# Optimization experiments

Measured on AMD Instinct MI355X. Metric: run time of the kernel, lower is better.

Reference implementation:

```python
import jax, jax.numpy as jnp
import numpy as np

N = 50000


def gcn_conv(x, edge_index, W, b):
    # PyG GCNConv: h = XW; add self-loops; sym-normalized scatter-add; + bias
    n = x.shape[0]
    h = x @ W  # [N, out]
    loop = jnp.arange(n)
    src = jnp.concatenate([edge_index[0], loop])
    dst = jnp.concatenate([edge_index[1], loop])
    deg = jax.ops.segment_sum(jnp.ones_like(dst, dtype=h.dtype), dst, num_segments=n)
    dinv = jax.lax.rsqrt(jnp.maximum(deg, 1.0))  # deg >= 1 after self-loops
    norm = dinv[src] * dinv[dst]  # [E+N]
    msg = h[src] * norm[:, None]  # [E+N, out]
    return jax.ops.segment_sum(msg, dst, num_segments=n) + b


def setup_inputs() -> dict:
    key = jax.random.key(0)
    ks = jax.random.split(key, 20)
    E = 1600000
    inp = {
        "metadata_a": jax.random.normal(ks[0], (N, 512), jnp.float32),
        "metadata_b": jax.random.normal(ks[1], (N, 512), jnp.float32),
        "x_a": jax.random.normal(ks[2], (N, 256), jnp.float32),
        "x_b": jax.random.normal(ks[3], (N, 256), jnp.float32),
        "edge_index_a": jax.random.randint(ks[4], (2, E), 0, N, dtype=jnp.int64),
        "edge_index_b": jax.random.randint(ks[5], (2, E), 0, N, dtype=jnp.int64),
        # parameters (fan-in scaled)
        "fc1_W": jax.random.normal(ks[6], (512, 128), jnp.float32) / np.sqrt(512),
        "fc1_b": jnp.zeros((128,), jnp.float32),
        "fc2_W": jax.random.normal(ks[7], (128, 128), jnp.float32) / np.sqrt(128),
        "fc2_b": jnp.zeros((128,), jnp.float32),
        "gcn1_W": jax.random.normal(ks[8], (256, 128), jnp.float32) / np.sqrt(256),
        "gcn1_b": jnp.zeros((128,), jnp.float32),
        "gcn2_W": jax.random.normal(ks[9], (128, 128), jnp.float32) / np.sqrt(128),
        "gcn2_b": jnp.zeros((128,), jnp.float32),
        "fcc_W": jax.random.normal(ks[10], (512, 128), jnp.float32) / np.sqrt(512),
        "fcc_b": jnp.zeros((128,), jnp.float32),
        "out_W": jax.random.normal(ks[11], (128, 1), jnp.float32) / np.sqrt(128),
        "out_b": jnp.zeros((1,), jnp.float32),
    }
    return inp


def reference(metadata_a, metadata_b, x_a, x_b, edge_index_a, edge_index_b,
              fc1_W, fc1_b, fc2_W, fc2_b, gcn1_W, gcn1_b, gcn2_W, gcn2_b,
              fcc_W, fcc_b, out_W, out_b):
    def mlp(m):
        m = jax.nn.relu(m @ fc1_W + fc1_b)
        return jax.nn.relu(m @ fc2_W + fc2_b)

    def gcn_branch(x, ei):
        x = jax.nn.relu(gcn_conv(x, ei, gcn1_W, gcn1_b))
        return jax.nn.relu(gcn_conv(x, ei, gcn2_W, gcn2_b))

    ma = mlp(metadata_a)
    mb = mlp(metadata_b)
    ga = gcn_branch(x_a, edge_index_a)
    gb = gcn_branch(x_b, edge_index_b)
    combined = jnp.concatenate([ma, mb, ga, gb], axis=1)  # [N, 512]
    combined = jax.nn.relu(combined @ fcc_W + fcc_b)
    return jax.nn.sigmoid(combined @ out_W + out_b)  # [N, 1]
```

## Files before the change

### kernel.cpp

```cpp
#include <hip/hip_runtime.h>
#include <math.h>


typedef __attribute__((ext_vector_type(8))) short bf16x8;
typedef __attribute__((ext_vector_type(4))) float f32x4;

static __device__ __forceinline__ unsigned short f2bf(float f) {
  unsigned u = __float_as_uint(f);
  unsigned r = u + 0x7fffu + ((u >> 16) & 1u);
  return (unsigned short)(r >> 16);
}
static __device__ __forceinline__ float bflo(unsigned m) { return __uint_as_float(m << 16); }
static __device__ __forceinline__ float bfhi(unsigned m) { return __uint_as_float(m & 0xffff0000u); }

static __device__ __forceinline__ bf16x8 cvt8(const float4& l, const float4& h) {
  bf16x8 a;
  a[0] = (short)f2bf(l.x); a[1] = (short)f2bf(l.y);
  a[2] = (short)f2bf(l.z); a[3] = (short)f2bf(l.w);
  a[4] = (short)f2bf(h.x); a[5] = (short)f2bf(h.y);
  a[6] = (short)f2bf(h.z); a[7] = (short)f2bf(h.w);
  return a;
}

static __device__ __forceinline__ void gl_lds16(const unsigned short* g, unsigned short* l) {
  __builtin_amdgcn_global_load_lds(
      (const __attribute__((address_space(1))) void*)g,
      (__attribute__((address_space(3))) void*)l, 16, 0, 0);
}

template <int KT>
__launch_bounds__(256)
__global__ void gemm_staged(const float* __restrict__ Av, const float* __restrict__ Av2,
                            int lda, const unsigned short* __restrict__ Wt,
                            const float* __restrict__ bias, const float* __restrict__ rowscale,
                            unsigned short* __restrict__ Cb, unsigned short* __restrict__ Cb2,
                            int ldc, int co, int co2, int Mh, int M, int do_relu) {
  static_assert(KT % 4 == 0, "KT multiple of 4");
  constexpr int NCH = KT / 4;
  __shared__ float4 As[2][2048];
  const int tid = threadIdx.x;
  const int wave = tid >> 6, lane = tid & 63, quad = lane >> 4, lr = lane & 15;
  const int m0 = blockIdx.x * 64 + wave * 16;
  const int mb = blockIdx.x * 64;

  f32x4 acc[8];
#pragma unroll
  for (int c = 0; c < 8; c++) acc[c] = (f32x4){0.f, 0.f, 0.f, 0.f};

  const int colq_src = (tid & 7) ^ ((tid >> 3) & 7);
  int r0g = mb + (tid >> 3);      if (r0g > M - 1) r0g = M - 1;
  int r1g = mb + 32 + (tid >> 3); if (r1g > M - 1) r1g = M - 1;
  const int h0 = r0g >= Mh, h1 = r1g >= Mh;
  const float* srcb0 = (h0 ? Av2 : Av) + (size_t)(r0g - (h0 ? Mh : 0)) * lda + colq_src * 4;
  const float* srcb1 = (h1 ? Av2 : Av) + (size_t)(r1g - (h1 ? Mh : 0)) * lda + colq_src * 4;

  auto stage = [&](int buf, int c0) {
#pragma unroll
    for (int s = 0; s < 8; s++) {
      const float* g = ((s & 1) ? srcb1 : srcb0) + (size_t)(c0 * 4 + (s >> 1)) * 32;
      gl_lds16((const unsigned short*)g,
               (unsigned short*)&As[buf][s * 256 + wave * 64]);
    }
  };

  const int h32 = wave >> 1;
  const int r5 = (wave & 1) * 16 + lr;
  const int swz = r5 & 7;
  const int fb_ = h32 * 256 + r5 * 8;

  const bf16x8* Bf = (const bf16x8*)Wt + lane;

  stage(0, 0);
  bf16x8 bb[2][8];
#pragma unroll
  for (int c = 0; c < 8; c++) bb[0][c] = Bf[c * 64];
  __builtin_amdgcn_sched_barrier(0);
  asm volatile("s_waitcnt vmcnt(0)" ::: "memory");
  __builtin_amdgcn_s_barrier();
  __builtin_amdgcn_sched_barrier(0);

  for (int ch = 0; ch < NCH; ch++) {
    if (ch + 1 < NCH) stage((ch + 1) & 1, ch + 1);
    const float4* cur = As[ch & 1];
#pragma unroll
    for (int kk = 0; kk < 4; kk++) {
      const int kt = ch * 4 + kk;
      float4 f0 = cur[kk * 512 + fb_ + ((2 * quad) ^ swz)];
      float4 f1 = cur[kk * 512 + fb_ + ((2 * quad + 1) ^ swz)];
      bf16x8 a = cvt8(f0, f1);
      if (kt + 1 < KT) {
        const bf16x8* Bk = Bf + (size_t)(kt + 1) * 512;
#pragma unroll
        for (int c = 0; c < 8; c++) bb[(kk + 1) & 1][c] = Bk[c * 64];
      }
#pragma unroll
      for (int c = 0; c < 8; c++)
        acc[c] = __builtin_amdgcn_mfma_f32_16x16x32_bf16(a, bb[kk & 1][c], acc[c], 0, 0, 0);
    }
    if (ch + 1 < NCH) {
      __builtin_amdgcn_sched_barrier(0);
      asm volatile("s_waitcnt vmcnt(0)" ::: "memory");
      __builtin_amdgcn_s_barrier();
      __builtin_amdgcn_sched_barrier(0);
    }
  }

  const int rbase = m0 + quad * 4;
  float rs[4];
#pragma unroll
  for (int i = 0; i < 4; i++) {
    int row = rbase + i;
    rs[i] = (rowscale && row < M) ? rowscale[row] : 1.0f;
  }
#pragma unroll
  for (int c = 0; c < 8; c++) {
    const int nc = c * 16 + lr;
    const float bi = bias ? bias[nc] : 0.f;
#pragma unroll
    for (int i = 0; i < 4; i++) {
      int row = rbase + i;
      if (row < M) {
        int hh = row >= Mh;
        int rr = row - (hh ? Mh : 0);
        float v = acc[c][i] * rs[i] + bi;
        if (do_relu) v = fmaxf(v, 0.f);
        unsigned short* C = hh ? Cb2 : Cb;
        C[(size_t)rr * ldc + (hh ? co2 : co) + nc] = f2bf(v);
      }
    }
  }
}

__launch_bounds__(256)
__global__ void gemm_reg4(const unsigned short* __restrict__ Av, const unsigned short* __restrict__ Av2,
                          int lda, const unsigned short* __restrict__ Wt,
                          const float* __restrict__ bias, const float* __restrict__ rowscale,
                          unsigned short* __restrict__ Cb, unsigned short* __restrict__ Cb2,
                          int ldc, int co, int co2, int Mh, int M, int do_relu) {
  const int tid = threadIdx.x;
  const int wave = tid >> 6, lane = tid & 63, quad = lane >> 4, lr = lane & 15;
  const int m0 = blockIdx.x * 64 + wave * 16;

  f32x4 acc[8];
#pragma unroll
  for (int c = 0; c < 8; c++) acc[c] = (f32x4){0.f, 0.f, 0.f, 0.f};

  int rg = m0 + lr; if (rg > M - 1) rg = M - 1;
  const int h = rg >= Mh;
  const unsigned short* aph = (h ? Av2 : Av) + (size_t)(rg - (h ? Mh : 0)) * lda + quad * 8;
  const bf16x8* Bf = (const bf16x8*)Wt + lane;

  bf16x8 hb[4];
#pragma unroll
  for (int k = 0; k < 4; k++) hb[k] = *(const bf16x8*)(aph + (size_t)k * 32);

  bf16x8 bb[2][8];
#pragma unroll
  for (int c = 0; c < 8; c++) bb[0][c] = Bf[c * 64];

#pragma unroll
  for (int kt = 0; kt < 4; kt++) {
    if (kt + 1 < 4) {
      const bf16x8* Bk = Bf + (size_t)(kt + 1) * 512;
#pragma unroll
      for (int c = 0; c < 8; c++) bb[(kt + 1) & 1][c] = Bk[c * 64];
    }
#pragma unroll
    for (int c = 0; c < 8; c++)
      acc[c] = __builtin_amdgcn_mfma_f32_16x16x32_bf16(hb[kt], bb[kt & 1][c], acc[c], 0, 0, 0);
  }

  const int rbase = m0 + quad * 4;
  float rs[4];
#pragma unroll
  for (int i = 0; i < 4; i++) {
    int row = rbase + i;
    rs[i] = (rowscale && row < M) ? rowscale[row] : 1.0f;
  }
#pragma unroll
  for (int c = 0; c < 8; c++) {
    const int nc = c * 16 + lr;
    const float bi = bias ? bias[nc] : 0.f;
#pragma unroll
    for (int i = 0; i < 4; i++) {
      int row = rbase + i;
      if (row < M) {
        int hh = row >= Mh;
        int rr = row - (hh ? Mh : 0);
        float v = acc[c][i] * rs[i] + bi;
        if (do_relu) v = fmaxf(v, 0.f);
        unsigned short* C = hh ? Cb2 : Cb;
        C[(size_t)rr * ldc + (hh ? co2 : co) + nc] = f2bf(v);
      }
    }
  }
}

__launch_bounds__(256)
__global__ void gemm_head(const unsigned short* __restrict__ A,
                          const unsigned short* __restrict__ Wt,
                          const float* __restrict__ bias,
                          const float* __restrict__ outW, const float* __restrict__ outb,
                          float* __restrict__ y, int M) {
  constexpr int KT = 16;
  const int tid = threadIdx.x;
  const int wave = tid >> 6, lane = tid & 63, quad = lane >> 4, lr = lane & 15;
  const int m0 = blockIdx.x * 64 + wave * 16;

  f32x4 acc[8];
#pragma unroll
  for (int c = 0; c < 8; c++) acc[c] = (f32x4){0.f, 0.f, 0.f, 0.f};

  int rg = m0 + lr; if (rg > M - 1) rg = M - 1;
  const unsigned short* aph = A + (size_t)rg * 512 + quad * 8;
  const bf16x8* Bf = (const bf16x8*)Wt + lane;

  bf16x8 hb[2][4];
#define LOADH(SLOT, BT)                                                     \
  if ((BT) < 4) {                                                           \
    _Pragma("unroll")                                                       \
    for (int kk = 0; kk < 4; kk++)                                          \
      hb[SLOT][kk] = *(const bf16x8*)(aph + (size_t)((BT) * 4 + kk) * 32);  \
  }
  LOADH(0, 0)
  LOADH(1, 1)

  bf16x8 bb[2][8];
#pragma unroll
  for (int c = 0; c < 8; c++) bb[0][c] = Bf[c * 64];

#pragma unroll
  for (int bt = 0; bt < 4; bt++) {
#pragma unroll
    for (int kk = 0; kk < 4; kk++) {
      const int kt = bt * 4 + kk;
      bf16x8 a = hb[bt & 1][kk];
      if (kt + 1 < KT) {
        const bf16x8* Bk = Bf + (size_t)(kt + 1) * 512;
#pragma unroll
        for (int c = 0; c < 8; c++) bb[(kk + 1) & 1][c] = Bk[c * 64];
      }
      if (kk == 3) { LOADH(bt & 1, bt + 2) }
#pragma unroll
      for (int c = 0; c < 8; c++)
        acc[c] = __builtin_amdgcn_mfma_f32_16x16x32_bf16(a, bb[kk & 1][c], acc[c], 0, 0, 0);
    }
  }
#undef LOADH

  float part[4] = {0.f, 0.f, 0.f, 0.f};
#pragma unroll
  for (int c = 0; c < 8; c++) {
    const int nc = c * 16 + lr;
    float w = outW[nc];
    float bi = bias[nc];
#pragma unroll
    for (int i = 0; i < 4; i++) part[i] += fmaxf(acc[c][i] + bi, 0.f) * w;
  }
#pragma unroll
  for (int i = 0; i < 4; i++) {
    part[i] += __shfl_xor(part[i], 1, 64);
    part[i] += __shfl_xor(part[i], 2, 64);
    part[i] += __shfl_xor(part[i], 4, 64);
    part[i] += __shfl_xor(part[i], 8, 64);
  }
  if (lr == 0) {
    const float ob = outb[0];
#pragma unroll
    for (int i = 0; i < 4; i++) {
      int row = m0 + quad * 4 + i;
      if (row < M) y[row] = 1.f / (1.f + expf(-(part[i] + ob)));
    }
  }
}

__global__ void prep_w(const float* __restrict__ fc1, const float* __restrict__ fc2,
                       const float* __restrict__ g1, const float* __restrict__ g2,
                       const float* __restrict__ fcc, unsigned short* __restrict__ wt) {
  int t = blockIdx.x * 256 + threadIdx.x;
  const float* src[5] = {fc1, fc2, g1, g2, fcc};
  const int Ks[5] = {512, 128, 256, 128, 512};
  int off = 0;
#pragma unroll
  for (int w = 0; w < 5; w++) {
    int K = Ks[w];
    int ngroups = K * 16;
    if (t < ngroups) {
      int lane = t & 63;
      int c = (t >> 6) & 7;
      int kt = t >> 9;
      int quad = lane >> 4, lr = lane & 15;
      int n = c * 16 + lr;
      unsigned short* dst = wt + off + (size_t)t * 8;
      const float* s = src[w];
#pragma unroll
      for (int j = 0; j < 8; j++) {
        int k = kt * 32 + quad * 8 + j;
        dst[j] = f2bf(s[k * 128 + n]);
      }
    }
    off += K * 128;
  }
}

__global__ void init_csr(int* __restrict__ gcur, int NB, int BCAP) {
  int i = blockIdx.x * 256 + threadIdx.x;
  if (i < 2 * NB) gcur[i] = i * BCAP;
}

__launch_bounds__(256)
__global__ void bucket_scatter(const int* __restrict__ eiA, const int* __restrict__ eiB,
                               int E, int T, int NB, int* __restrict__ gcur,
                               unsigned* __restrict__ records) {
  __shared__ unsigned staging[4096];
  __shared__ int hist[129];
  __shared__ int offs[129];
  __shared__ int gbase[128];
  __shared__ int sm[128];
  const int g = blockIdx.x >= T;
  const int tile = blockIdx.x - g * T;
  const int* ei = g ? eiB : eiA;
  const int tid = threadIdx.x;
  for (int i = tid; i <= NB; i += 256) hist[i] = 0;
  __syncthreads();
  const int base = tile * 4096;
  int myb[16], myp[16];
  unsigned myrec[16];
#pragma unroll
  for (int j = 0; j < 16; j++) {
    int li = base + j * 256 + tid;
    int b = NB;
    unsigned rec = 0;
    if (li < E) {
      int s = ei[li], d = ei[E + li];
      b = d >> 9;
      rec = (unsigned)s | ((unsigned)d << 16);
    }
    myb[j] = b; myrec[j] = rec;
    myp[j] = atomicAdd(&hist[b], 1);
  }
  __syncthreads();
  if (tid < 128) sm[tid] = (tid <= NB) ? hist[tid] : 0;
  __syncthreads();
  for (int d = 1; d < 128; d <<= 1) {
    int v = 0;
    if (tid < 128) { v = sm[tid]; if (tid >= d) v += sm[tid - d]; }
    __syncthreads();
    if (tid < 128) sm[tid] = v;
    __syncthreads();
  }
  if (tid < 128) offs[tid] = sm[tid] - ((tid <= NB) ? hist[tid] : 0);
  __syncthreads();
#pragma unroll
  for (int j = 0; j < 16; j++)
    if (myb[j] < NB) staging[offs[myb[j]] + myp[j]] = myrec[j];
  if (tid < NB && hist[tid] > 0) gbase[tid] = atomicAdd(&gcur[g * NB + tid], hist[tid]);
  __syncthreads();
  const int total = offs[NB];
  for (int i = tid; i < total; i += 256) {
    unsigned rec = staging[i];
    int b = (int)(rec >> 16) >> 9;
    records[gbase[b] + (i - offs[b])] = rec;
  }
}

__launch_bounds__(256)
__global__ void csr_build(const unsigned* __restrict__ records, const int* __restrict__ gcur,
                          int N, int NB, int BCAP,
                          int2* __restrict__ rpA, int2* __restrict__ rpB,
                          float* __restrict__ dinv, unsigned short* __restrict__ csrAll) {
  __shared__ int ncnt[512];
  __shared__ int excl[512];
  __shared__ int sm[256];
  const int g = blockIdx.x >= NB;
  const int b = blockIdx.x - g * NB;
  const int tid = threadIdx.x;
  const int R = (g * NB + b) * BCAP;
  const int cnt = gcur[g * NB + b] - R;
  const int node0 = b << 9;
  const int nb = min(512, N - node0);
  const unsigned* rec = records + R;
  int2* rp = g ? rpB : rpA;
  unsigned short* csr = csrAll + (size_t)g * NB * BCAP;

  for (int i = tid; i < 512; i += 256) ncnt[i] = 0;
  __syncthreads();
  for (int i = tid; i < cnt; i += 256)
    atomicAdd(&ncnt[(rec[i] >> 16) & 511], 1);
  __syncthreads();
  int a0 = ncnt[2 * tid], a1 = ncnt[2 * tid + 1];
  int ps = a0 + a1;
  sm[tid] = ps;
  __syncthreads();
  for (int d = 1; d < 256; d <<= 1) {
    int v = sm[tid];
    if (tid >= d) v += sm[tid - d];
    __syncthreads();
    sm[tid] = v;
    __syncthreads();
  }
  int e0 = sm[tid] - ps;
  excl[2 * tid] = e0;
  excl[2 * tid + 1] = e0 + a0;
  __syncthreads();
  for (int i = tid; i < nb; i += 256) {
    int s = b * BCAP + excl[i];
    rp[node0 + i] = make_int2(s, s + ncnt[i]);
    dinv[g * N + node0 + i] = rsqrtf((float)(ncnt[i] + 1));
  }
  __syncthreads();
  for (int i = tid; i < 512; i += 256) ncnt[i] = excl[i];
  __syncthreads();
  for (int i = tid; i < cnt; i += 256) {
    unsigned r = rec[i];
    int p = atomicAdd(&ncnt[(r >> 16) & 511], 1);
    csr[b * BCAP + p] = (unsigned short)(r & 0xffffu);
  }
}

struct f2x4 { float2 a, b, c, d; };
static __device__ __forceinline__ void acc2(f2x4& A, const uint4& m) {
  A.a.x += bflo(m.x); A.a.y += bfhi(m.x);
  A.b.x += bflo(m.y); A.b.y += bfhi(m.y);
  A.c.x += bflo(m.z); A.c.y += bfhi(m.z);
  A.d.x += bflo(m.w); A.d.y += bfhi(m.w);
}

__launch_bounds__(256)
__global__ void gather16(const unsigned short* __restrict__ hsA,
                         const unsigned short* __restrict__ hsB,
                         const unsigned short* __restrict__ csrA,
                         const unsigned short* __restrict__ csrB,
                         const int2* __restrict__ rpA, const int2* __restrict__ rpB,
                         const float* __restrict__ dinv,
                         const float* __restrict__ bias,
                         unsigned short* __restrict__ outA, unsigned short* __restrict__ outB,
                         int ldA, int coA, int ldB, int coB, int N) {
  int widx = (blockIdx.x * 256 + threadIdx.x) >> 6;
  if (widx >= 2 * N) return;
  int g = widx >= N;
  int v = g ? widx - N : widx;
  const unsigned short* hs = g ? hsB : hsA;
  const unsigned short* csr = g ? csrB : csrA;
  int2 se = (g ? rpB : rpA)[v];
  unsigned short* out = g ? outB : outA;
  const int ldc = g ? ldB : ldA;
  const int co = g ? coB : coA;
  const int lane = threadIdx.x & 63;
  const int grp = lane >> 4;
  const int u = lane & 15;
  const unsigned short* rowb = hs + u * 8;

  f2x4 A0 = {{0,0},{0,0},{0,0},{0,0}};
  f2x4 A1 = {{0,0},{0,0},{0,0},{0,0}};

  int e = se.x;
  const int end = se.y;
  for (; e + 16 <= end; e += 16) {
    int s0 = csr[e + grp];
    int s1 = csr[e + 4 + grp];
    int s2 = csr[e + 8 + grp];
    int s3 = csr[e + 12 + grp];
    uint4 m0 = *(const uint4*)(rowb + (size_t)s0 * 128);
    uint4 m1 = *(const uint4*)(rowb + (size_t)s1 * 128);
    uint4 m2 = *(const uint4*)(rowb + (size_t)s2 * 128);
    uint4 m3 = *(const uint4*)(rowb + (size_t)s3 * 128);
    acc2(A0, m0); acc2(A1, m1); acc2(A0, m2); acc2(A1, m3);
  }
  for (; e + 4 <= end; e += 4) {
    int s0 = csr[e + grp];
    uint4 m0 = *(const uint4*)(rowb + (size_t)s0 * 128);
    acc2(A0, m0);
  }
  int r = end - e;
  if (r > 0) {
    int s0 = csr[e + (grp < r ? grp : r - 1)];
    uint4 m = *(const uint4*)(rowb + (size_t)s0 * 128);
    float msk = (grp < r) ? 1.f : 0.f;
    A1.a.x = fmaf(msk, bflo(m.x), A1.a.x); A1.a.y = fmaf(msk, bfhi(m.x), A1.a.y);
    A1.b.x = fmaf(msk, bflo(m.y), A1.b.x); A1.b.y = fmaf(msk, bfhi(m.y), A1.b.y);
    A1.c.x = fmaf(msk, bflo(m.z), A1.c.x); A1.c.y = fmaf(msk, bfhi(m.z), A1.c.y);
    A1.d.x = fmaf(msk, bflo(m.w), A1.d.x); A1.d.y = fmaf(msk, bfhi(m.w), A1.d.y);
  }

  float acc[8] = {A0.a.x + A1.a.x, A0.a.y + A1.a.y, A0.b.x + A1.b.x, A0.b.y + A1.b.y,
                  A0.c.x + A1.c.x, A0.c.y + A1.c.y, A0.d.x + A1.d.x, A0.d.y + A1.d.y};
#pragma unroll
  for (int j = 0; j < 8; j++) {
    acc[j] += __shfl_down(acc[j], 32, 64);
    acc[j] += __shfl_down(acc[j], 16, 64);
  }
  if (grp == 0) {
    uint4 smv = *(const uint4*)(rowb + (size_t)v * 128);
    acc[0] += bflo(smv.x); acc[1] += bfhi(smv.x);
    acc[2] += bflo(smv.y); acc[3] += bfhi(smv.y);
    acc[4] += bflo(smv.z); acc[5] += bfhi(smv.z);
    acc[6] += bflo(smv.w); acc[7] += bfhi(smv.w);
    float dv = dinv[g * N + v];
    float4 b0 = *(const float4*)(bias + u * 8);
    float4 b1 = *(const float4*)(bias + u * 8 + 4);
    float o0 = fmaxf(acc[0] * dv + b0.x, 0.f), o1 = fmaxf(acc[1] * dv + b0.y, 0.f);
    float o2 = fmaxf(acc[2] * dv + b0.z, 0.f), o3 = fmaxf(acc[3] * dv + b0.w, 0.f);
    float o4 = fmaxf(acc[4] * dv + b1.x, 0.f), o5 = fmaxf(acc[5] * dv + b1.y, 0.f);
    float o6 = fmaxf(acc[6] * dv + b1.z, 0.f), o7 = fmaxf(acc[7] * dv + b1.w, 0.f);
    uint4 P;
    P.x = (unsigned)f2bf(o0) | ((unsigned)f2bf(o1) << 16);
    P.y = (unsigned)f2bf(o2) | ((unsigned)f2bf(o3) << 16);
    P.z = (unsigned)f2bf(o4) | ((unsigned)f2bf(o5) << 16);
    P.w = (unsigned)f2bf(o6) | ((unsigned)f2bf(o7) << 16);
    *(uint4*)(out + (size_t)v * ldc + co + u * 8) = P;
  }
}

extern "C" void kernel_launch(void* const* d_in, const int* in_sizes, int n_in,
                              void* d_out, int out_size, void* d_ws, size_t ws_size,
                              hipStream_t stream) {
  const float* meta_a = (const float*)d_in[0];
  const float* meta_b = (const float*)d_in[1];
  const float* x_a    = (const float*)d_in[2];
  const float* x_b    = (const float*)d_in[3];
  const int*   ei_a   = (const int*)d_in[4];
  const int*   ei_b   = (const int*)d_in[5];
  const float* fc1_W = (const float*)d_in[6];
  const float* fc1_b = (const float*)d_in[7];
  const float* fc2_W = (const float*)d_in[8];
  const float* fc2_b = (const float*)d_in[9];
  const float* gcn1_W = (const float*)d_in[10];
  const float* gcn1_b = (const float*)d_in[11];
  const float* gcn2_W = (const float*)d_in[12];
  const float* gcn2_b = (const float*)d_in[13];
  const float* fcc_W = (const float*)d_in[14];
  const float* fcc_b = (const float*)d_in[15];
  const float* out_W = (const float*)d_in[16];
  const float* out_b = (const float*)d_in[17];
  float* y = (float*)d_out;

  const int N = in_sizes[0] / 512;
  const int E = in_sizes[4] / 2;
  const int NB = (N + 511) >> 9;
  const int T = (E + 4095) / 4096;
  const int BCAP = 17408;

  char* p = (char*)d_ws;
  auto alloc = [&](size_t bytes) { char* r = p; p += (bytes + 255) & ~255ull; return r; };
  unsigned short* combined = (unsigned short*)alloc((size_t)N * 512 * 2);
  unsigned short* t0 = (unsigned short*)alloc((size_t)N * 128 * 2);
  unsigned short* t1 = (unsigned short*)alloc((size_t)N * 128 * 2);
  unsigned short* t2 = (unsigned short*)alloc((size_t)N * 128 * 2);
  unsigned short* t3 = (unsigned short*)alloc((size_t)N * 128 * 2);
  unsigned short* wt = (unsigned short*)alloc(196608 * 2);
  float* dinv = (float*)alloc((size_t)2 * N * 4);
  int2* rpA = (int2*)alloc((size_t)N * 8);
  int2* rpB = (int2*)alloc((size_t)N * 8);
  int* gcur = (int*)alloc((size_t)2 * NB * 4);
  unsigned* records = (unsigned*)alloc((size_t)2 * NB * BCAP * 4 + 4096);
  unsigned short* csrAll = (unsigned short*)alloc((size_t)2 * NB * BCAP * 2 + 4096);
  unsigned short* csrA = csrAll;
  unsigned short* csrB = csrAll + (size_t)NB * BCAP;

  unsigned short* wt_fc1 = wt;
  unsigned short* wt_fc2 = wt + 65536;
  unsigned short* wt_g1  = wt + 81920;
  unsigned short* wt_g2  = wt + 114688;
  unsigned short* wt_fcc = wt + 131072;

  const int grid1 = (N + 63) / 64;
  const int grid2 = (2 * N + 63) / 64;

  prep_w<<<32, 256, 0, stream>>>(fc1_W, fc2_W, gcn1_W, gcn2_W, fcc_W, wt);
  init_csr<<<1, 256, 0, stream>>>(gcur, NB, BCAP);
  bucket_scatter<<<2 * T, 256, 0, stream>>>(ei_a, ei_b, E, T, NB, gcur, records);
  csr_build<<<2 * NB, 256, 0, stream>>>(records, gcur, N, NB, BCAP, rpA, rpB, dinv, csrAll);

  gemm_staged<16><<<grid2, 256, 0, stream>>>(meta_a, meta_b, 512, wt_fc1, fc1_b, nullptr,
                                             t0, t1, 128, 0, 0, N, 2 * N, 1);
  gemm_reg4<<<grid2, 256, 0, stream>>>(t0, t1, 128, wt_fc2, fc2_b, nullptr,
                                       combined, combined, 512, 0, 128, N, 2 * N, 1);

  gemm_staged<8><<<grid2, 256, 0, stream>>>(x_a, x_b, 256, wt_g1, nullptr, dinv,
                                            t0, t1, 128, 0, 0, N, 2 * N, 0);
  gather16<<<(2 * N + 3) / 4, 256, 0, stream>>>(t0, t1, csrA, csrB, rpA, rpB, dinv, gcn1_b,
                                                t2, t3, 128, 0, 128, 0, N);
  gemm_reg4<<<grid2, 256, 0, stream>>>(t2, t3, 128, wt_g2, nullptr, dinv,
                                       t0, t1, 128, 0, 0, N, 2 * N, 0);
  gather16<<<(2 * N + 3) / 4, 256, 0, stream>>>(t0, t1, csrA, csrB, rpA, rpB, dinv, gcn2_b,
                                                combined, combined, 512, 256, 512, 384, N);

  gemm_head<<<grid1, 256, 0, stream>>>(combined, wt_fcc, fcc_b, out_W, out_b, y, N);
}
```

Before: 745.8 us.

## Unify GEMMs into 128-row tile kernel staging weights in LDS

Replaces the two GEMM kernels with one templated kernel. Each wave now computes two 16-row tiles (128 rows per block). Weight chunks are staged into LDS via global_load_lds and shared across waves, while A rows are loaded straight into registers and prefetched one chunk ahead. This reuses each B fragment across two MFMA tiles and cuts global weight traffic per row, at the cost of more registers (launch bounds hint of 3 blocks) and fewer blocks in the grid.

```diff
diff --git a/kernel.cpp b/kernel.cpp
--- a/kernel.cpp
+++ b/kernel.cpp
@@ -28,169 +28,131 @@
       (__attribute__((address_space(3))) void*)l, 16, 0, 0);
 }
 
-template <int KT>
-__launch_bounds__(256)
-__global__ void gemm_staged(const float* __restrict__ Av, const float* __restrict__ Av2,
-                            int lda, const unsigned short* __restrict__ Wt,
-                            const float* __restrict__ bias, const float* __restrict__ rowscale,
-                            unsigned short* __restrict__ Cb, unsigned short* __restrict__ Cb2,
-                            int ldc, int co, int co2, int Mh, int M, int do_relu) {
-  static_assert(KT % 4 == 0, "KT multiple of 4");
-  constexpr int NCH = KT / 4;
-  __shared__ float4 As[2][2048];
-  const int tid = threadIdx.x;
-  const int wave = tid >> 6, lane = tid & 63, quad = lane >> 4, lr = lane & 15;
-  const int m0 = blockIdx.x * 64 + wave * 16;
-  const int mb = blockIdx.x * 64;
-
-  f32x4 acc[8];
-#pragma unroll
-  for (int c = 0; c < 8; c++) acc[c] = (f32x4){0.f, 0.f, 0.f, 0.f};
-
-  const int colq_src = (tid & 7) ^ ((tid >> 3) & 7);
-  int r0g = mb + (tid >> 3);      if (r0g > M - 1) r0g = M - 1;
-  int r1g = mb + 32 + (tid >> 3); if (r1g > M - 1) r1g = M - 1;
-  const int h0 = r0g >= Mh, h1 = r1g >= Mh;
-  const float* srcb0 = (h0 ? Av2 : Av) + (size_t)(r0g - (h0 ? Mh : 0)) * lda + colq_src * 4;
-  const float* srcb1 = (h1 ? Av2 : Av) + (size_t)(r1g - (h1 ? Mh : 0)) * lda + colq_src * 4;
-
-  auto stage = [&](int buf, int c0) {
-#pragma unroll
-    for (int s = 0; s < 8; s++) {
-      const float* g = ((s & 1) ? srcb1 : srcb0) + (size_t)(c0 * 4 + (s >> 1)) * 32;
-      gl_lds16((const unsigned short*)g,
-               (unsigned short*)&As[buf][s * 256 + wave * 64]);
-    }
-  };
-
-  const int h32 = wave >> 1;
-  const int r5 = (wave & 1) * 16 + lr;
-  const int swz = r5 & 7;
-  const int fb_ = h32 * 256 + r5 * 8;
-
-  const bf16x8* Bf = (const bf16x8*)Wt + lane;
-
-  stage(0, 0);
-  bf16x8 bb[2][8];
-#pragma unroll
-  for (int c = 0; c < 8; c++) bb[0][c] = Bf[c * 64];
-  __builtin_amdgcn_sched_barrier(0);
-  asm volatile("s_waitcnt vmcnt(0)" ::: "memory");
-  __builtin_amdgcn_s_barrier();
-  __builtin_amdgcn_sched_barrier(0);
-
-  for (int ch = 0; ch < NCH; ch++) {
-    if (ch + 1 < NCH) stage((ch + 1) & 1, ch + 1);
-    const float4* cur = As[ch & 1];
-#pragma unroll
-    for (int kk = 0; kk < 4; kk++) {
-      const int kt = ch * 4 + kk;
-      float4 f0 = cur[kk * 512 + fb_ + ((2 * quad) ^ swz)];
-      float4 f1 = cur[kk * 512 + fb_ + ((2 * quad + 1) ^ swz)];
-      bf16x8 a = cvt8(f0, f1);
-      if (kt + 1 < KT) {
-        const bf16x8* Bk = Bf + (size_t)(kt + 1) * 512;
-#pragma unroll
-        for (int c = 0; c < 8; c++) bb[(kk + 1) & 1][c] = Bk[c * 64];
-      }
-#pragma unroll
-      for (int c = 0; c < 8; c++)
-        acc[c] = __builtin_amdgcn_mfma_f32_16x16x32_bf16(a, bb[kk & 1][c], acc[c], 0, 0, 0);
-    }
-    if (ch + 1 < NCH) {
-      __builtin_amdgcn_sched_barrier(0);
-      asm volatile("s_waitcnt vmcnt(0)" ::: "memory");
-      __builtin_amdgcn_s_barrier();
-      __builtin_amdgcn_sched_barrier(0);
-    }
-  }
-
-  const int rbase = m0 + quad * 4;
-  float rs[4];
-#pragma unroll
-  for (int i = 0; i < 4; i++) {
-    int row = rbase + i;
-    rs[i] = (rowscale && row < M) ? rowscale[row] : 1.0f;
-  }
-#pragma unroll
-  for (int c = 0; c < 8; c++) {
-    const int nc = c * 16 + lr;
-    const float bi = bias ? bias[nc] : 0.f;
-#pragma unroll
-    for (int i = 0; i < 4; i++) {
-      int row = rbase + i;
-      if (row < M) {
-        int hh = row >= Mh;
-        int rr = row - (hh ? Mh : 0);
-        float v = acc[c][i] * rs[i] + bi;
-        if (do_relu) v = fmaxf(v, 0.f);
-        unsigned short* C = hh ? Cb2 : Cb;
-        C[(size_t)rr * ldc + (hh ? co2 : co) + nc] = f2bf(v);
-      }
-    }
-  }
-}
-
-__launch_bounds__(256)
-__global__ void gemm_reg4(const unsigned short* __restrict__ Av, const unsigned short* __restrict__ Av2,
+template <int AFP32, int KT>
+__launch_bounds__(256, 3)
+__global__ void gemm_tile(const void* __restrict__ Av, const void* __restrict__ Av2,
                           int lda, const unsigned short* __restrict__ Wt,
                           const float* __restrict__ bias, const float* __restrict__ rowscale,
                           unsigned short* __restrict__ Cb, unsigned short* __restrict__ Cb2,
                           int ldc, int co, int co2, int Mh, int M, int do_relu) {
+  static_assert(KT % 4 == 0, "KT multiple of 4");
+  constexpr int NCH = KT / 4;
+  constexpr int NBUF = (NCH > 1) ? 2 : 1;
+  __shared__ unsigned short Bs[NBUF][16384];
   const int tid = threadIdx.x;
   const int wave = tid >> 6, lane = tid & 63, quad = lane >> 4, lr = lane & 15;
-  const int m0 = blockIdx.x * 64 + wave * 16;
-
-  f32x4 acc[8];
-#pragma unroll
-  for (int c = 0; c < 8; c++) acc[c] = (f32x4){0.f, 0.f, 0.f, 0.f};
-
-  int rg = m0 + lr; if (rg > M - 1) rg = M - 1;
-  const int h = rg >= Mh;
-  const unsigned short* aph = (h ? Av2 : Av) + (size_t)(rg - (h ? Mh : 0)) * lda + quad * 8;
-  const bf16x8* Bf = (const bf16x8*)Wt + lane;
-
-  bf16x8 hb[4];
-#pragma unroll
-  for (int k = 0; k < 4; k++) hb[k] = *(const bf16x8*)(aph + (size_t)k * 32);
-
-  bf16x8 bb[2][8];
-#pragma unroll
-  for (int c = 0; c < 8; c++) bb[0][c] = Bf[c * 64];
-
-#pragma unroll
-  for (int kt = 0; kt < 4; kt++) {
-    if (kt + 1 < 4) {
-      const bf16x8* Bk = Bf + (size_t)(kt + 1) * 512;
-#pragma unroll
-      for (int c = 0; c < 8; c++) bb[(kt + 1) & 1][c] = Bk[c * 64];
-    }
-#pragma unroll
-    for (int c = 0; c < 8; c++)
-      acc[c] = __builtin_amdgcn_mfma_f32_16x16x32_bf16(hb[kt], bb[kt & 1][c], acc[c], 0, 0, 0);
-  }
-
-  const int rbase = m0 + quad * 4;
-  float rs[4];
-#pragma unroll
-  for (int i = 0; i < 4; i++) {
-    int row = rbase + i;
-    rs[i] = (rowscale && row < M) ? rowscale[row] : 1.0f;
-  }
-#pragma unroll
-  for (int c = 0; c < 8; c++) {
-    const int nc = c * 16 + lr;
-    const float bi = bias ? bias[nc] : 0.f;
+  const int m0 = blockIdx.x * 128 + wave * 32;
+
+  f32x4 acc[2][8];
+#pragma unroll
+  for (int t = 0; t < 2; t++)
+#pragma unroll
+    for (int c = 0; c < 8; c++) acc[t][c] = (f32x4){0.f, 0.f, 0.f, 0.f};
+
+  const float* apf[2];
+  const unsigned short* aph[2];
+#pragma unroll
+  for (int t = 0; t < 2; t++) {
+    int rg = m0 + t * 16 + lr; if (rg > M - 1) rg = M - 1;
+    const int h = rg >= Mh;
+    const size_t rl = (size_t)(rg - (h ? Mh : 0));
+    if (AFP32) apf[t] = (const float*)(h ? Av2 : Av) + rl * lda + quad * 8;
+    else       aph[t] = (const unsigned short*)(h ? Av2 : Av) + rl * lda + quad * 8;
+  }
+
+  auto stage = [&](int b, int ch) {
+    const unsigned short* g = Wt + ((size_t)ch * 4 + wave) * 4096 + lane * 8;
+    unsigned short* l = &Bs[b][wave * 4096];
+#pragma unroll
+    for (int i = 0; i < 8; i++)
+      gl_lds16(g + i * 512, l + i * 512);
+  };
+
+  stage(0, 0);
+  __builtin_amdgcn_sched_barrier(0);
+  float4 pl[4][2], ph[4][2];
+  bf16x8 pa[4][2];
+#pragma unroll
+  for (int d = 0; d < 4; d++) {
+#pragma unroll
+    for (int t = 0; t < 2; t++) {
+      if (AFP32) {
+        pl[d][t] = *(const float4*)(apf[t] + (size_t)d * 32);
+        ph[d][t] = *(const float4*)(apf[t] + (size_t)d * 32 + 4);
+      } else {
+        pa[d][t] = *(const bf16x8*)(aph[t] + (size_t)d * 32);
+      }
+    }
+  }
+  __builtin_amdgcn_sched_barrier(0);
+  if (AFP32) asm volatile("s_waitcnt vmcnt(16)" ::: "memory");
+  else       asm volatile("s_waitcnt vmcnt(8)" ::: "memory");
+  __builtin_amdgcn_s_barrier();
+  __builtin_amdgcn_sched_barrier(0);
+
+#pragma unroll
+  for (int ch = 0; ch < NCH; ch++) {
+    if (ch + 1 < NCH) {
+      stage((ch + 1) & 1, ch + 1);
+      __builtin_amdgcn_sched_barrier(0);
+    }
+#pragma unroll
+    for (int kk = 0; kk < 4; kk++) {
+      const int kt = ch * 4 + kk;
+      bf16x8 a0, a1;
+      if (AFP32) { a0 = cvt8(pl[kk][0], ph[kk][0]); a1 = cvt8(pl[kk][1], ph[kk][1]); }
+      else       { a0 = pa[kk][0]; a1 = pa[kk][1]; }
+      if (kt + 4 < KT) {
+#pragma unroll
+        for (int t = 0; t < 2; t++) {
+          if (AFP32) {
+            pl[kk][t] = *(const float4*)(apf[t] + (size_t)(kt + 4) * 32);
+            ph[kk][t] = *(const float4*)(apf[t] + (size_t)(kt + 4) * 32 + 4);
+          } else {
+            pa[kk][t] = *(const bf16x8*)(aph[t] + (size_t)(kt + 4) * 32);
+          }
+        }
+      }
+#pragma unroll
+      for (int c = 0; c < 8; c++) {
+        bf16x8 b = *(const bf16x8*)&Bs[ch & (NBUF - 1)][kk * 4096 + c * 512 + lane * 8];
+        acc[0][c] = __builtin_amdgcn_mfma_f32_16x16x32_bf16(a0, b, acc[0][c], 0, 0, 0);
+        acc[1][c] = __builtin_amdgcn_mfma_f32_16x16x32_bf16(a1, b, acc[1][c], 0, 0, 0);
+      }
+    }
+    if (ch + 1 < NCH) {
+      __builtin_amdgcn_sched_barrier(0);
+      if (AFP32) asm volatile("s_waitcnt vmcnt(16)" ::: "memory");
+      else       asm volatile("s_waitcnt vmcnt(8)" ::: "memory");
+      __builtin_amdgcn_s_barrier();
+      __builtin_amdgcn_sched_barrier(0);
+    }
+  }
+
+#pragma unroll
+  for (int t = 0; t < 2; t++) {
+    const int rbase = m0 + t * 16 + quad * 4;
+    float rs[4];
 #pragma unroll
     for (int i = 0; i < 4; i++) {
       int row = rbase + i;
-      if (row < M) {
-        int hh = row >= Mh;
-        int rr = row - (hh ? Mh : 0);
-        float v = acc[c][i] * rs[i] + bi;
-        if (do_relu) v = fmaxf(v, 0.f);
-        unsigned short* C = hh ? Cb2 : Cb;
-        C[(size_t)rr * ldc + (hh ? co2 : co) + nc] = f2bf(v);
+      rs[i] = (rowscale && row < M) ? rowscale[row] : 1.0f;
+    }
+#pragma unroll
+    for (int c = 0; c < 8; c++) {
+      const int nc = c * 16 + lr;
+      const float bi = bias ? bias[nc] : 0.f;
+#pragma unroll
+      for (int i = 0; i < 4; i++) {
+        int row = rbase + i;
+        if (row < M) {
+          int hh = row >= Mh;
+          int rr = row - (hh ? Mh : 0);
+          float v = acc[t][c][i] * rs[i] + bi;
+          if (do_relu) v = fmaxf(v, 0.f);
+          unsigned short* C = hh ? Cb2 : Cb;
+          C[(size_t)rr * ldc + (hh ? co2 : co) + nc] = f2bf(v);
+        }
       }
     }
   }
@@ -565,24 +527,24 @@
   unsigned short* wt_fcc = wt + 131072;
 
   const int grid1 = (N + 63) / 64;
-  const int grid2 = (2 * N + 63) / 64;
+  const int gridT = (2 * N + 127) / 128;
 
   prep_w<<<32, 256, 0, stream>>>(fc1_W, fc2_W, gcn1_W, gcn2_W, fcc_W, wt);
   init_csr<<<1, 256, 0, stream>>>(gcur, NB, BCAP);
   bucket_scatter<<<2 * T, 256, 0, stream>>>(ei_a, ei_b, E, T, NB, gcur, records);
   csr_build<<<2 * NB, 256, 0, stream>>>(records, gcur, N, NB, BCAP, rpA, rpB, dinv, csrAll);
 
-  gemm_staged<16><<<grid2, 256, 0, stream>>>(meta_a, meta_b, 512, wt_fc1, fc1_b, nullptr,
-                                             t0, t1, 128, 0, 0, N, 2 * N, 1);
-  gemm_reg4<<<grid2, 256, 0, stream>>>(t0, t1, 128, wt_fc2, fc2_b, nullptr,
-                                       combined, combined, 512, 0, 128, N, 2 * N, 1);
-
-  gemm_staged<8><<<grid2, 256, 0, stream>>>(x_a, x_b, 256, wt_g1, nullptr, dinv,
-                                            t0, t1, 128, 0, 0, N, 2 * N, 0);
+  gemm_tile<1, 16><<<gridT, 256, 0, stream>>>(meta_a, meta_b, 512, wt_fc1, fc1_b, nullptr,
+                                              t0, t1, 128, 0, 0, N, 2 * N, 1);
+  gemm_tile<0, 4><<<gridT, 256, 0, stream>>>(t0, t1, 128, wt_fc2, fc2_b, nullptr,
+                                             combined, combined, 512, 0, 128, N, 2 * N, 1);
+
+  gemm_tile<1, 8><<<gridT, 256, 0, stream>>>(x_a, x_b, 256, wt_g1, nullptr, dinv,
+                                             t0, t1, 128, 0, 0, N, 2 * N, 0);
   gather16<<<(2 * N + 3) / 4, 256, 0, stream>>>(t0, t1, csrA, csrB, rpA, rpB, dinv, gcn1_b,
                                                 t2, t3, 128, 0, 128, 0, N);
-  gemm_reg4<<<grid2, 256, 0, stream>>>(t2, t3, 128, wt_g2, nullptr, dinv,
-                                       t0, t1, 128, 0, 0, N, 2 * N, 0);
+  gemm_tile<0, 4><<<gridT, 256, 0, stream>>>(t2, t3, 128, wt_g2, nullptr, dinv,
+                                             t0, t1, 128, 0, 0, N, 2 * N, 0);
   gather16<<<(2 * N + 3) / 4, 256, 0, stream>>>(t0, t1, csrA, csrB, rpA, rpB, dinv, gcn2_b,
                                                 combined, combined, 512, 256, 512, 384, N);
 
```

After: 753.3 us. Within noise of the previous version (+1.0%).
